# Optimization experiments

Measured on AMD Instinct MI355X. Metric: run time of the kernel, lower is better.

The kernel has to match this reference:

```python
import jax, jax.numpy as jnp
import numpy as np

N_NODES = 100000
HIDDEN = 256
N_MOVES = 500000
N_GRAPHS = 512
EPS = 1e-16  # matches pyg softmax denominator eps


def setup_inputs() -> dict:
    key = jax.random.key(0)
    k1, k2, k3, k4, k5, k6, k7 = jax.random.split(key, 7)
    node_embeddings = jax.random.normal(k1, (N_NODES, HIDDEN), dtype=jnp.float32)
    legal_moves = jax.random.randint(k2, (2, N_MOVES), 0, N_NODES, dtype=jnp.int64)
    batch = jnp.sort(jax.random.randint(k3, (N_NODES,), 0, N_GRAPHS, dtype=jnp.int64))
    # MLP params: Linear(2h, h) -> ReLU -> Linear(h, 1)
    s1 = 1.0 / np.sqrt(2 * HIDDEN)
    s2 = 1.0 / np.sqrt(HIDDEN)
    W1 = jax.random.uniform(k4, (2 * HIDDEN, HIDDEN), jnp.float32, -s1, s1)
    b1 = jax.random.uniform(k5, (HIDDEN,), jnp.float32, -s1, s1)
    W2 = jax.random.uniform(k6, (HIDDEN, 1), jnp.float32, -s2, s2)
    b2 = jax.random.uniform(k7, (1,), jnp.float32, -s2, s2)
    return {"node_embeddings": node_embeddings, "legal_moves": legal_moves,
            "batch": batch, "W1": W1, "b1": b1, "W2": W2, "b2": b2}


def reference(node_embeddings, legal_moves, batch, W1, b1, W2, b2):
    sources = legal_moves[0]
    targets = legal_moves[1]
    # gather endpoints and concat -> [E, 2h]
    move_features = jnp.concatenate(
        [node_embeddings[sources], node_embeddings[targets]], axis=-1)
    h = jax.nn.relu(move_features @ W1 + b1)          # [E, h]
    logits = jnp.squeeze(h @ W2 + b2, axis=-1)        # [E]
    # segment softmax over the graph each move's source node belongs to
    move_batch = batch[sources]                        # [E]
    seg_max = jax.ops.segment_max(logits, move_batch, num_segments=N_GRAPHS)
    ex = jnp.exp(logits - seg_max[move_batch])
    seg_sum = jax.ops.segment_sum(ex, move_batch, num_segments=N_GRAPHS)
    probs = ex / (seg_sum[move_batch] + EPS)
    return probs
```

## Files before the change

### kernel.cpp

```cpp
#include <hip/hip_runtime.h>
#include <hip/hip_bf16.h>

#define NNODES 100000
#define HID 256
#define NMOVES 500000
#define NGRAPHS 512
#define BM 128
#define BN 32
#define PB 128

typedef __attribute__((ext_vector_type(8))) short short8;
typedef __attribute__((ext_vector_type(4))) float f32x4;

#define AS_GLOBAL __attribute__((address_space(1)))
#define AS_LDS __attribute__((address_space(3)))

__device__ __forceinline__ unsigned f2bf(float f) {
    unsigned u = __builtin_bit_cast(unsigned, f);
    u += 0x7FFFu + ((u >> 16) & 1u);
    return u >> 16;
}
__device__ __forceinline__ float bf2f(ushort h) {
    unsigned u = ((unsigned)h) << 16;
    return __builtin_bit_cast(float, u);
}
__device__ __forceinline__ unsigned encf(float f) {
    unsigned b = __builtin_bit_cast(unsigned, f);
    return (b & 0x80000000u) ? ~b : (b ^ 0x80000000u);
}
__device__ __forceinline__ float decf(unsigned u) {
    unsigned b = (u & 0x80000000u) ? (u ^ 0x80000000u) : ~u;
    return __builtin_bit_cast(float, b);
}

__global__ void k_convert_w1(const float* __restrict__ W1, ushort* __restrict__ W1t) {
    int t = blockIdx.x * blockDim.x + threadIdx.x;
    int n = t >> 8, k = t & 255;
    float v = (n < 256) ? W1[k * 256 + n] : W1[(k + 256) * 256 + (n - 256)];
    W1t[t] = (ushort)f2bf(v);
}

__global__ __launch_bounds__(512, 4) void k_gemm(const float* __restrict__ emb,
                                                 const ushort* __restrict__ Bt,
                                                 ushort* __restrict__ P, int M) {
    __shared__ __align__(16) char lds[65536];
    int tid = threadIdx.x;
    int lane = tid & 63;
    int wave = tid >> 6;
    int tm = blockIdx.x * BM;
    int wm = wave >> 1;
    int wn = wave & 1;
    int fr = lane & 15;
    int q = lane >> 4;
    int sw = fr & 7;

#pragma unroll
    for (int i = 0; i < 8; ++i) {
        int cid = i * 512 + tid;
        int row = cid >> 5;
        int j = cid & 31;
        int grow = tm + row; if (grow >= M) grow = M - 1;
        const float4* sp = reinterpret_cast<const float4*>(emb + (size_t)grow * 256 + (j << 3));
        float4 v0 = sp[0], v1 = sp[1];
        uint4 o;
        o.x = f2bf(v0.x) | (f2bf(v0.y) << 16);
        o.y = f2bf(v0.z) | (f2bf(v0.w) << 16);
        o.z = f2bf(v1.x) | (f2bf(v1.y) << 16);
        o.w = f2bf(v1.z) | (f2bf(v1.w) << 16);
        *reinterpret_cast<uint4*>(lds + row * 512 + ((j ^ (row & 7)) << 4)) = o;
    }
    __syncthreads();

    short8 af[2][8];
#pragma unroll
    for (int m = 0; m < 2; ++m) {
        int row = wm * 32 + m * 16 + fr;
#pragma unroll
        for (int kt = 0; kt < 8; ++kt)
            af[m][kt] = *reinterpret_cast<const short8*>(
                lds + row * 512 + (((kt * 4 + q) ^ sw) << 4));
    }
    __syncthreads();

#define STAGE(STRIP, BUFI)                                                          \
    {                                                                               \
        int tn2 = (STRIP) * BN;                                                     \
        _Pragma("unroll")                                                           \
        for (int i = 0; i < 2; ++i) {                                               \
            int cid = i * 512 + tid;                                                \
            int row = cid >> 5, c = cid & 31;                                       \
            const ushort* src = Bt + (size_t)(tn2 + row) * 256 + ((c ^ (row & 7)) << 3); \
            __builtin_amdgcn_global_load_lds((const AS_GLOBAL void*)src,            \
                (AS_LDS void*)(lds + (BUFI) * 16384 + (i * 512 + wave * 64) * 16),  \
                16, 0, 0);                                                          \
        }                                                                           \
    }

    STAGE(0, 0);
    STAGE(1, 1);

#pragma unroll 1
    for (int r = 0; r < 16; ++r) {
        if (r == 0)      asm volatile("s_waitcnt vmcnt(2)" ::: "memory");
        else if (r < 15) asm volatile("s_waitcnt vmcnt(10)" ::: "memory");
        else             asm volatile("s_waitcnt vmcnt(8)" ::: "memory");
        asm volatile("s_barrier" ::: "memory");

        const char* bp = lds + (r & 1) * 16384;
        f32x4 acc0 = {0.f, 0.f, 0.f, 0.f};
        f32x4 acc1 = {0.f, 0.f, 0.f, 0.f};
#pragma unroll
        for (int kt = 0; kt < 8; ++kt) {
            short8 bf = *reinterpret_cast<const short8*>(
                bp + (wn * 16 + fr) * 512 + (((kt * 4 + q) ^ sw) << 4));
            acc0 = __builtin_amdgcn_mfma_f32_16x16x32_bf16(af[0][kt], bf, acc0, 0, 0, 0);
            acc1 = __builtin_amdgcn_mfma_f32_16x16x32_bf16(af[1][kt], bf, acc1, 0, 0, 0);
        }
        int pcol = r * BN + wn * 16 + fr;
#pragma unroll
        for (int j = 0; j < 4; ++j) {
            int prow0 = tm + wm * 32 + q * 4 + j;
            if (prow0 < M) P[(size_t)prow0 * 512 + pcol] = (ushort)f2bf(acc0[j]);
            int prow1 = prow0 + 16;
            if (prow1 < M) P[(size_t)prow1 * 512 + pcol] = (ushort)f2bf(acc1[j]);
        }

        asm volatile("s_barrier" ::: "memory");
        if (r < 14) STAGE(r + 2, (r & 1));
    }
#undef STAGE
}

__device__ __forceinline__ float dot8(uint4 a, uint4 b, const float* b1v, const float* w2v, int o) {
    unsigned aw[4] = {a.x, a.y, a.z, a.w};
    unsigned bw[4] = {b.x, b.y, b.z, b.w};
    float r = 0.f;
#pragma unroll
    for (int i = 0; i < 4; ++i) {
        float a0 = bf2f((ushort)(aw[i] & 0xffffu));
        float a1 = bf2f((ushort)(aw[i] >> 16));
        float c0 = bf2f((ushort)(bw[i] & 0xffffu));
        float c1 = bf2f((ushort)(bw[i] >> 16));
        float h0 = fmaxf(a0 + c0 + b1v[o + 2 * i], 0.f);
        float h1 = fmaxf(a1 + c1 + b1v[o + 2 * i + 1], 0.f);
        r += h0 * w2v[o + 2 * i] + h1 * w2v[o + 2 * i + 1];
    }
    return r;
}

__global__ __launch_bounds__(256) void k_moves(const int* __restrict__ srcs,
                                               const int* __restrict__ tgts,
                                               const int* __restrict__ batch,
                                               const ushort* __restrict__ P,
                                               const float* __restrict__ b1,
                                               const float* __restrict__ W2,
                                               const float* __restrict__ b2,
                                               float* __restrict__ logits,
                                               int* __restrict__ mb) {
    int tid = threadIdx.x;
    int lane = tid & 63;
    int sub = lane >> 4;
    int ch = lane & 15;

    float b1v[16], w2v[16];
    const float4* b1p = reinterpret_cast<const float4*>(b1);
    const float4* w2p = reinterpret_cast<const float4*>(W2);
#pragma unroll
    for (int q = 0; q < 4; ++q) {
        float4 bv = b1p[ch * 4 + q];
        float4 wv = w2p[ch * 4 + q];
        b1v[q * 4 + 0] = bv.x; b1v[q * 4 + 1] = bv.y; b1v[q * 4 + 2] = bv.z; b1v[q * 4 + 3] = bv.w;
        w2v[q * 4 + 0] = wv.x; w2v[q * 4 + 1] = wv.y; w2v[q * 4 + 2] = wv.z; w2v[q * 4 + 3] = wv.w;
    }
    float b2s = b2[0];

    int wid = (blockIdx.x * 256 + tid) >> 6;
    int nw = (gridDim.x * 256) >> 6;

    for (int base = wid * 8; base < NMOVES; base += nw * 8) {
        int m0 = base + sub;
        int m1 = base + 4 + sub;
        int s0 = srcs[m0], t0 = tgts[m0];
        int s1 = srcs[m1], t1 = tgts[m1];
        const uint4* pa0 = reinterpret_cast<const uint4*>(P + (size_t)s0 * 512 + ch * 16);
        const uint4* pb0 = reinterpret_cast<const uint4*>(P + (size_t)t0 * 512 + 256 + ch * 16);
        const uint4* pa1 = reinterpret_cast<const uint4*>(P + (size_t)s1 * 512 + ch * 16);
        const uint4* pb1 = reinterpret_cast<const uint4*>(P + (size_t)t1 * 512 + 256 + ch * 16);
        uint4 a00 = pa0[0], a01 = pa0[1];
        uint4 c00 = pb0[0], c01 = pb0[1];
        uint4 a10 = pa1[0], a11 = pa1[1];
        uint4 c10 = pb1[0], c11 = pb1[1];
        int g0 = batch[s0];
        int g1 = batch[s1];

        float p0 = dot8(a00, c00, b1v, w2v, 0) + dot8(a01, c01, b1v, w2v, 8);
        float p1 = dot8(a10, c10, b1v, w2v, 0) + dot8(a11, c11, b1v, w2v, 8);
#pragma unroll
        for (int off = 1; off < 16; off <<= 1) {
            p0 += __shfl_xor(p0, off);
            p1 += __shfl_xor(p1, off);
        }
        if (ch == 0) {
            logits[m0] = p0 + b2s; mb[m0] = g0;
            logits[m1] = p1 + b2s; mb[m1] = g1;
        }
    }
}

__global__ __launch_bounds__(256) void k_part(const float* __restrict__ logits,
                                              const int* __restrict__ mb,
                                              float* __restrict__ pmax,
                                              float* __restrict__ psum) {
    __shared__ unsigned lmax[NGRAPHS];
    __shared__ float lsum[NGRAPHS];
    int tid = threadIdx.x;
    lmax[tid] = 0u; lmax[tid + 256] = 0u;
    lsum[tid] = 0.f; lsum[tid + 256] = 0.f;
    __syncthreads();

    const int NV = NMOVES / 4;
    int stride = PB * 256;
    for (int v = blockIdx.x * 256 + tid; v < NV; v += stride) {
        float4 l = reinterpret_cast<const float4*>(logits)[v];
        int4 g = reinterpret_cast<const int4*>(mb)[v];
        atomicMax(&lmax[g.x], encf(l.x));
        atomicMax(&lmax[g.y], encf(l.y));
        atomicMax(&lmax[g.z], encf(l.z));
        atomicMax(&lmax[g.w], encf(l.w));
    }
    __syncthreads();
    for (int v = blockIdx.x * 256 + tid; v < NV; v += stride) {
        float4 l = reinterpret_cast<const float4*>(logits)[v];
        int4 g = reinterpret_cast<const int4*>(mb)[v];
        atomicAdd(&lsum[g.x], __expf(l.x - decf(lmax[g.x])));
        atomicAdd(&lsum[g.y], __expf(l.y - decf(lmax[g.y])));
        atomicAdd(&lsum[g.z], __expf(l.z - decf(lmax[g.z])));
        atomicAdd(&lsum[g.w], __expf(l.w - decf(lmax[g.w])));
    }
    __syncthreads();

#pragma unroll
    for (int i = 0; i < 2; ++i) {
        int s = tid + i * 256;
        unsigned e = lmax[s];
        pmax[blockIdx.x * NGRAPHS + s] = (e == 0u) ? -INFINITY : decf(e);
        psum[blockIdx.x * NGRAPHS + s] = lsum[s];
    }
}

__global__ __launch_bounds__(64) void k_combine(const float* __restrict__ pmax,
                                                const float* __restrict__ psum,
                                                float* __restrict__ gmax,
                                                float* __restrict__ ginv) {
    int s = blockIdx.x;
    int lane = threadIdx.x;
    float pm0 = pmax[lane * NGRAPHS + s];
    float pm1 = pmax[(lane + 64) * NGRAPHS + s];
    float ps0 = psum[lane * NGRAPHS + s];
    float ps1 = psum[(lane + 64) * NGRAPHS + s];
    float M = fmaxf(pm0, pm1);
#pragma unroll
    for (int off = 32; off; off >>= 1) M = fmaxf(M, __shfl_xor(M, off));
    float S = (ps0 > 0.f ? ps0 * __expf(pm0 - M) : 0.f)
            + (ps1 > 0.f ? ps1 * __expf(pm1 - M) : 0.f);
#pragma unroll
    for (int off = 32; off; off >>= 1) S += __shfl_xor(S, off);
    if (lane == 0) {
        gmax[s] = M;
        ginv[s] = 1.f / (S + 1e-16f);
    }
}

__global__ void k_norm(const float* __restrict__ logits, const int* __restrict__ mb,
                       const float* __restrict__ gmax, const float* __restrict__ ginv,
                       float* __restrict__ out) {
    const int NV = NMOVES / 4;
    int i = blockIdx.x * blockDim.x + threadIdx.x;
    int n = gridDim.x * blockDim.x;
    for (int v = i; v < NV; v += n) {
        float4 l = reinterpret_cast<const float4*>(logits)[v];
        int4 g = reinterpret_cast<const int4*>(mb)[v];
        float4 o;
        o.x = __expf(l.x - gmax[g.x]) * ginv[g.x];
        o.y = __expf(l.y - gmax[g.y]) * ginv[g.y];
        o.z = __expf(l.z - gmax[g.z]) * ginv[g.z];
        o.w = __expf(l.w - gmax[g.w]) * ginv[g.w];
        reinterpret_cast<float4*>(out)[v] = o;
    }
}

extern "C" void kernel_launch(void* const* d_in, const int* in_sizes, int n_in,
                              void* d_out, int out_size, void* d_ws, size_t ws_size,
                              hipStream_t stream) {
    const float* emb = (const float*)d_in[0];
    const int* moves = (const int*)d_in[1];
    const int* batch = (const int*)d_in[2];
    const float* W1 = (const float*)d_in[3];
    const float* b1 = (const float*)d_in[4];
    const float* W2 = (const float*)d_in[5];
    const float* b2 = (const float*)d_in[6];
    float* out = (float*)d_out;

    auto al = [](size_t x) { return (x + 255) & ~(size_t)255; };
    char* ws = (char*)d_ws;
    size_t off = 0;
    ushort* W1t = (ushort*)(ws + off); off += al((size_t)512 * 256 * 2);
    ushort* P   = (ushort*)(ws + off); off += al((size_t)NNODES * 512 * 2);
    float* logits = (float*)(ws + off); off += al((size_t)NMOVES * 4);
    int* mb       = (int*)(ws + off);   off += al((size_t)NMOVES * 4);
    float* pmax   = (float*)(ws + off); off += al((size_t)PB * NGRAPHS * 4);
    float* psum   = (float*)(ws + off); off += al((size_t)PB * NGRAPHS * 4);
    float* gmax   = (float*)(ws + off); off += al((size_t)NGRAPHS * 4);
    float* ginv   = (float*)(ws + off); off += al((size_t)NGRAPHS * 4);

    k_convert_w1<<<512, 256, 0, stream>>>(W1, W1t);

    int tiles_m = (NNODES + BM - 1) / BM;
    k_gemm<<<tiles_m, 512, 0, stream>>>(emb, W1t, P, NNODES);

    k_moves<<<2048, 256, 0, stream>>>(moves, moves + NMOVES, batch, P, b1, W2, b2,
                                      logits, mb);
    k_part<<<PB, 256, 0, stream>>>(logits, mb, pmax, psum);
    k_combine<<<NGRAPHS, 64, 0, stream>>>(pmax, psum, gmax, ginv);
    k_norm<<<512, 256, 0, stream>>>(logits, mb, gmax, ginv, out);
}
```

Before: 146.9 us.

## Restage GEMM with 128-wide B strips, register-loaded A, and packed transposed stores

```diff
diff --git a/kernel.cpp b/kernel.cpp
--- a/kernel.cpp
+++ b/kernel.cpp
@@ -6,7 +6,6 @@
 #define NMOVES 500000
 #define NGRAPHS 512
 #define BM 128
-#define BN 32
 #define PB 128
 
 typedef __attribute__((ext_vector_type(8))) short short8;
@@ -40,10 +39,10 @@
     W1t[t] = (ushort)f2bf(v);
 }
 
-__global__ __launch_bounds__(512, 4) void k_gemm(const float* __restrict__ emb,
+__global__ __launch_bounds__(512, 2) void k_gemm(const float* __restrict__ emb,
                                                  const ushort* __restrict__ Bt,
                                                  ushort* __restrict__ P, int M) {
-    __shared__ __align__(16) char lds[65536];
+    __shared__ __align__(16) char lds[131072];
     int tid = threadIdx.x;
     int lane = tid & 63;
     int wave = tid >> 6;
@@ -54,80 +53,108 @@
     int q = lane >> 4;
     int sw = fr & 7;
 
-#pragma unroll
-    for (int i = 0; i < 8; ++i) {
-        int cid = i * 512 + tid;
-        int row = cid >> 5;
-        int j = cid & 31;
-        int grow = tm + row; if (grow >= M) grow = M - 1;
-        const float4* sp = reinterpret_cast<const float4*>(emb + (size_t)grow * 256 + (j << 3));
-        float4 v0 = sp[0], v1 = sp[1];
-        uint4 o;
-        o.x = f2bf(v0.x) | (f2bf(v0.y) << 16);
-        o.y = f2bf(v0.z) | (f2bf(v0.w) << 16);
-        o.z = f2bf(v1.x) | (f2bf(v1.y) << 16);
-        o.w = f2bf(v1.z) | (f2bf(v1.w) << 16);
-        *reinterpret_cast<uint4*>(lds + row * 512 + ((j ^ (row & 7)) << 4)) = o;
-    }
-    __syncthreads();
-
-    short8 af[2][8];
-#pragma unroll
-    for (int m = 0; m < 2; ++m) {
-        int row = wm * 32 + m * 16 + fr;
-#pragma unroll
-        for (int kt = 0; kt < 8; ++kt)
-            af[m][kt] = *reinterpret_cast<const short8*>(
-                lds + row * 512 + (((kt * 4 + q) ^ sw) << 4));
-    }
-    __syncthreads();
-
 #define STAGE(STRIP, BUFI)                                                          \
     {                                                                               \
-        int tn2 = (STRIP) * BN;                                                     \
         _Pragma("unroll")                                                           \
-        for (int i = 0; i < 2; ++i) {                                               \
-            int cid = i * 512 + tid;                                                \
+        for (int i = 0; i < 8; ++i) {                                               \
+            int cid = i * 512 + tid;                         \
             int row = cid >> 5, c = cid & 31;                                       \
-            const ushort* src = Bt + (size_t)(tn2 + row) * 256 + ((c ^ (row & 7)) << 3); \
+            const ushort* src = Bt + (size_t)((STRIP) * 128 + row) * 256            \
+                                   + ((c ^ (row & 7)) << 3);                        \
             __builtin_amdgcn_global_load_lds((const AS_GLOBAL void*)src,            \
-                (AS_LDS void*)(lds + (BUFI) * 16384 + (i * 512 + wave * 64) * 16),  \
-                16, 0, 0);                                                          \
+                (AS_LDS void*)(lds + (BUFI) * 65536 + cid * 16), 16, 0, 0);         \
         }                                                                           \
     }
 
     STAGE(0, 0);
     STAGE(1, 1);
 
-#pragma unroll 1
-    for (int r = 0; r < 16; ++r) {
-        if (r == 0)      asm volatile("s_waitcnt vmcnt(2)" ::: "memory");
-        else if (r < 15) asm volatile("s_waitcnt vmcnt(10)" ::: "memory");
-        else             asm volatile("s_waitcnt vmcnt(8)" ::: "memory");
-        asm volatile("s_barrier" ::: "memory");
-
-        const char* bp = lds + (r & 1) * 16384;
-        f32x4 acc0 = {0.f, 0.f, 0.f, 0.f};
-        f32x4 acc1 = {0.f, 0.f, 0.f, 0.f};
+    short8 af[2][8];
+#pragma unroll
+    for (int m = 0; m < 2; ++m) {
+        int grow = tm + wm * 32 + m * 16 + fr;
+        if (grow >= M) grow = M - 1;
+        const float* base = emb + (size_t)grow * 256;
 #pragma unroll
         for (int kt = 0; kt < 8; ++kt) {
-            short8 bf = *reinterpret_cast<const short8*>(
-                bp + (wn * 16 + fr) * 512 + (((kt * 4 + q) ^ sw) << 4));
-            acc0 = __builtin_amdgcn_mfma_f32_16x16x32_bf16(af[0][kt], bf, acc0, 0, 0, 0);
-            acc1 = __builtin_amdgcn_mfma_f32_16x16x32_bf16(af[1][kt], bf, acc1, 0, 0, 0);
+            float4 v0 = *reinterpret_cast<const float4*>(base + (kt * 4 + q) * 8);
+            float4 v1 = *reinterpret_cast<const float4*>(base + (kt * 4 + q) * 8 + 4);
+            short8 f;
+            f[0] = (short)f2bf(v0.x); f[1] = (short)f2bf(v0.y);
+            f[2] = (short)f2bf(v0.z); f[3] = (short)f2bf(v0.w);
+            f[4] = (short)f2bf(v1.x); f[5] = (short)f2bf(v1.y);
+            f[6] = (short)f2bf(v1.z); f[7] = (short)f2bf(v1.w);
+            af[m][kt] = f;
         }
-        int pcol = r * BN + wn * 16 + fr;
-#pragma unroll
-        for (int j = 0; j < 4; ++j) {
-            int prow0 = tm + wm * 32 + q * 4 + j;
-            if (prow0 < M) P[(size_t)prow0 * 512 + pcol] = (ushort)f2bf(acc0[j]);
-            int prow1 = prow0 + 16;
-            if (prow1 < M) P[(size_t)prow1 * 512 + pcol] = (ushort)f2bf(acc1[j]);
+    }
+
+    f32x4 acc[4][4][2];
+#pragma unroll
+    for (int r = 0; r < 4; ++r)
+#pragma unroll
+        for (int n = 0; n < 4; ++n)
+#pragma unroll
+            for (int m = 0; m < 2; ++m) acc[r][n][m] = (f32x4){0.f, 0.f, 0.f, 0.f};
+
+#define STRIP_COMPUTE(R)                                                            \
+    {                                                                               \
+        const char* bp = lds + ((R) & 1) * 65536;                                   \
+        _Pragma("unroll")                                                           \
+        for (int kt = 0; kt < 8; ++kt) {                                            \
+            short8 bf[4];                                                           \
+            _Pragma("unroll")                                                       \
+            for (int n = 0; n < 4; ++n)                                             \
+                bf[n] = *reinterpret_cast<const short8*>(                           \
+                    bp + (wn * 64 + n * 16 + fr) * 512 + (((kt * 4 + q) ^ sw) << 4)); \
+            _Pragma("unroll")                                                       \
+            for (int n = 0; n < 4; ++n) {                                           \
+                acc[R][n][0] = __builtin_amdgcn_mfma_f32_16x16x32_bf16(             \
+                    bf[n], af[0][kt], acc[R][n][0], 0, 0, 0);                       \
+                acc[R][n][1] = __builtin_amdgcn_mfma_f32_16x16x32_bf16(             \
+                    bf[n], af[1][kt], acc[R][n][1], 0, 0, 0);                       \
+            }                                                                       \
+        }                                                                           \
+    }
+
+    asm volatile("s_waitcnt vmcnt(8)" ::: "memory");
+    asm volatile("s_barrier" ::: "memory");
+    STRIP_COMPUTE(0);
+    asm volatile("s_barrier" ::: "memory");
+    STAGE(2, 0);
+
+    asm volatile("s_waitcnt vmcnt(8)" ::: "memory");
+    asm volatile("s_barrier" ::: "memory");
+    STRIP_COMPUTE(1);
+    asm volatile("s_barrier" ::: "memory");
+    STAGE(3, 1);
+
+    asm volatile("s_waitcnt vmcnt(8)" ::: "memory");
+    asm volatile("s_barrier" ::: "memory");
+    STRIP_COMPUTE(2);
+    asm volatile("s_barrier" ::: "memory");
+
+    asm volatile("s_waitcnt vmcnt(0)" ::: "memory");
+    asm volatile("s_barrier" ::: "memory");
+    STRIP_COMPUTE(3);
+
+#pragma unroll
+    for (int r = 0; r < 4; ++r) {
+#pragma unroll
+        for (int m = 0; m < 2; ++m) {
+            int prow = tm + wm * 32 + m * 16 + fr;
+            if (prow < M) {
+#pragma unroll
+                for (int n = 0; n < 4; ++n) {
+                    int pcol = r * 128 + wn * 64 + n * 16 + q * 4;
+                    uint2 pk;
+                    pk.x = f2bf(acc[r][n][m][0]) | (f2bf(acc[r][n][m][1]) << 16);
+                    pk.y = f2bf(acc[r][n][m][2]) | (f2bf(acc[r][n][m][3]) << 16);
+                    *reinterpret_cast<uint2*>(P + (size_t)prow * 512 + pcol) = pk;
+                }
+            }
         }
-
-        asm volatile("s_barrier" ::: "memory");
-        if (r < 14) STAGE(r + 2, (r & 1));
-    }
+    }
+#undef STRIP_COMPUTE
 #undef STAGE
 }
 
```

New measurement: 184.6 us. 1.26x slower.

## Load A fragments directly from global, halve LDS, swap MFMA operands for packed stores

Applied to the files above, without the earlier changes.

```diff
diff --git a/kernel.cpp b/kernel.cpp
--- a/kernel.cpp
+++ b/kernel.cpp
@@ -40,10 +40,10 @@
     W1t[t] = (ushort)f2bf(v);
 }
 
-__global__ __launch_bounds__(512, 4) void k_gemm(const float* __restrict__ emb,
+__global__ __launch_bounds__(512, 8) void k_gemm(const float* __restrict__ emb,
                                                  const ushort* __restrict__ Bt,
                                                  ushort* __restrict__ P, int M) {
-    __shared__ __align__(16) char lds[65536];
+    __shared__ __align__(16) char lds[32768];
     int tid = threadIdx.x;
     int lane = tid & 63;
     int wave = tid >> 6;
@@ -54,42 +54,14 @@
     int q = lane >> 4;
     int sw = fr & 7;
 
-#pragma unroll
-    for (int i = 0; i < 8; ++i) {
-        int cid = i * 512 + tid;
-        int row = cid >> 5;
-        int j = cid & 31;
-        int grow = tm + row; if (grow >= M) grow = M - 1;
-        const float4* sp = reinterpret_cast<const float4*>(emb + (size_t)grow * 256 + (j << 3));
-        float4 v0 = sp[0], v1 = sp[1];
-        uint4 o;
-        o.x = f2bf(v0.x) | (f2bf(v0.y) << 16);
-        o.y = f2bf(v0.z) | (f2bf(v0.w) << 16);
-        o.z = f2bf(v1.x) | (f2bf(v1.y) << 16);
-        o.w = f2bf(v1.z) | (f2bf(v1.w) << 16);
-        *reinterpret_cast<uint4*>(lds + row * 512 + ((j ^ (row & 7)) << 4)) = o;
-    }
-    __syncthreads();
-
-    short8 af[2][8];
-#pragma unroll
-    for (int m = 0; m < 2; ++m) {
-        int row = wm * 32 + m * 16 + fr;
-#pragma unroll
-        for (int kt = 0; kt < 8; ++kt)
-            af[m][kt] = *reinterpret_cast<const short8*>(
-                lds + row * 512 + (((kt * 4 + q) ^ sw) << 4));
-    }
-    __syncthreads();
-
 #define STAGE(STRIP, BUFI)                                                          \
     {                                                                               \
-        int tn2 = (STRIP) * BN;                                                     \
         _Pragma("unroll")                                                           \
         for (int i = 0; i < 2; ++i) {                                               \
-            int cid = i * 512 + tid;                                                \
+            int cid = i * 512 + tid;                         \
             int row = cid >> 5, c = cid & 31;                                       \
-            const ushort* src = Bt + (size_t)(tn2 + row) * 256 + ((c ^ (row & 7)) << 3); \
+            const ushort* src = Bt + (size_t)((STRIP) * BN + row) * 256             \
+                                   + ((c ^ (row & 7)) << 3);                        \
             __builtin_amdgcn_global_load_lds((const AS_GLOBAL void*)src,            \
                 (AS_LDS void*)(lds + (BUFI) * 16384 + (i * 512 + wave * 64) * 16),  \
                 16, 0, 0);                                                          \
@@ -99,11 +71,29 @@
     STAGE(0, 0);
     STAGE(1, 1);
 
+    short8 af[2][8];
+#pragma unroll
+    for (int m = 0; m < 2; ++m) {
+        int grow = tm + wm * 32 + m * 16 + fr;
+        if (grow >= M) grow = M - 1;
+        const float* base = emb + (size_t)grow * 256;
+#pragma unroll
+        for (int kt = 0; kt < 8; ++kt) {
+            float4 v0 = *reinterpret_cast<const float4*>(base + (kt * 4 + q) * 8);
+            float4 v1 = *reinterpret_cast<const float4*>(base + (kt * 4 + q) * 8 + 4);
+            short8 f;
+            f[0] = (short)f2bf(v0.x); f[1] = (short)f2bf(v0.y);
+            f[2] = (short)f2bf(v0.z); f[3] = (short)f2bf(v0.w);
+            f[4] = (short)f2bf(v1.x); f[5] = (short)f2bf(v1.y);
+            f[6] = (short)f2bf(v1.z); f[7] = (short)f2bf(v1.w);
+            af[m][kt] = f;
+        }
+    }
+
 #pragma unroll 1
     for (int r = 0; r < 16; ++r) {
-        if (r == 0)      asm volatile("s_waitcnt vmcnt(2)" ::: "memory");
-        else if (r < 15) asm volatile("s_waitcnt vmcnt(10)" ::: "memory");
-        else             asm volatile("s_waitcnt vmcnt(8)" ::: "memory");
+        if (r < 15) asm volatile("s_waitcnt vmcnt(4)" ::: "memory");
+        else        asm volatile("s_waitcnt vmcnt(2)" ::: "memory");
         asm volatile("s_barrier" ::: "memory");
 
         const char* bp = lds + (r & 1) * 16384;
@@ -113,16 +103,23 @@
         for (int kt = 0; kt < 8; ++kt) {
             short8 bf = *reinterpret_cast<const short8*>(
                 bp + (wn * 16 + fr) * 512 + (((kt * 4 + q) ^ sw) << 4));
-            acc0 = __builtin_amdgcn_mfma_f32_16x16x32_bf16(af[0][kt], bf, acc0, 0, 0, 0);
-            acc1 = __builtin_amdgcn_mfma_f32_16x16x32_bf16(af[1][kt], bf, acc1, 0, 0, 0);
-        }
-        int pcol = r * BN + wn * 16 + fr;
-#pragma unroll
-        for (int j = 0; j < 4; ++j) {
-            int prow0 = tm + wm * 32 + q * 4 + j;
-            if (prow0 < M) P[(size_t)prow0 * 512 + pcol] = (ushort)f2bf(acc0[j]);
-            int prow1 = prow0 + 16;
-            if (prow1 < M) P[(size_t)prow1 * 512 + pcol] = (ushort)f2bf(acc1[j]);
+            acc0 = __builtin_amdgcn_mfma_f32_16x16x32_bf16(bf, af[0][kt], acc0, 0, 0, 0);
+            acc1 = __builtin_amdgcn_mfma_f32_16x16x32_bf16(bf, af[1][kt], acc1, 0, 0, 0);
+        }
+        int pcol = r * BN + wn * 16 + q * 4;
+        int prow0 = tm + wm * 32 + fr;
+        if (prow0 < M) {
+            uint2 pk;
+            pk.x = f2bf(acc0[0]) | (f2bf(acc0[1]) << 16);
+            pk.y = f2bf(acc0[2]) | (f2bf(acc0[3]) << 16);
+            *reinterpret_cast<uint2*>(P + (size_t)prow0 * 512 + pcol) = pk;
+        }
+        int prow1 = prow0 + 16;
+        if (prow1 < M) {
+            uint2 pk;
+            pk.x = f2bf(acc1[0]) | (f2bf(acc1[1]) << 16);
+            pk.y = f2bf(acc1[2]) | (f2bf(acc1[3]) << 16);
+            *reinterpret_cast<uint2*>(P + (size_t)prow1 * 512 + pcol) = pk;
         }
 
         asm volatile("s_barrier" ::: "memory");
```

After: 362.9 us. +147.1%, slower.

## Fuse per-block segment max/sum partials into move-logit kernel, drop k_part

Applied to the files above, without the earlier changes.

```diff
diff --git a/kernel.cpp b/kernel.cpp
--- a/kernel.cpp
+++ b/kernel.cpp
@@ -7,7 +7,7 @@
 #define NGRAPHS 512
 #define BM 128
 #define BN 32
-#define PB 128
+#define PBM 2048
 
 typedef __attribute__((ext_vector_type(8))) short short8;
 typedef __attribute__((ext_vector_type(4))) float f32x4;
@@ -84,12 +84,12 @@
 
 #define STAGE(STRIP, BUFI)                                                          \
     {                                                                               \
-        int tn2 = (STRIP) * BN;                                                     \
         _Pragma("unroll")                                                           \
         for (int i = 0; i < 2; ++i) {                                               \
-            int cid = i * 512 + tid;                                                \
+            int cid = i * 512 + tid;                         \
             int row = cid >> 5, c = cid & 31;                                       \
-            const ushort* src = Bt + (size_t)(tn2 + row) * 256 + ((c ^ (row & 7)) << 3); \
+            const ushort* src = Bt + (size_t)((STRIP) * BN + row) * 256             \
+                                   + ((c ^ (row & 7)) << 3);                        \
             __builtin_amdgcn_global_load_lds((const AS_GLOBAL void*)src,            \
                 (AS_LDS void*)(lds + (BUFI) * 16384 + (i * 512 + wave * 64) * 16),  \
                 16, 0, 0);                                                          \
@@ -156,11 +156,18 @@
                                                const float* __restrict__ W2,
                                                const float* __restrict__ b2,
                                                float* __restrict__ logits,
-                                               int* __restrict__ mb) {
+                                               int* __restrict__ mb,
+                                               float* __restrict__ pmax,
+                                               float* __restrict__ psum) {
+    __shared__ unsigned lmax[NGRAPHS];
+    __shared__ float lsum[NGRAPHS];
     int tid = threadIdx.x;
     int lane = tid & 63;
     int sub = lane >> 4;
     int ch = lane & 15;
+    lmax[tid] = 0u; lmax[tid + 256] = 0u;
+    lsum[tid] = 0.f; lsum[tid + 256] = 0.f;
+    __syncthreads();
 
     float b1v[16], w2v[16];
     const float4* b1p = reinterpret_cast<const float4*>(b1);
@@ -201,41 +208,21 @@
             p1 += __shfl_xor(p1, off);
         }
         if (ch == 0) {
-            logits[m0] = p0 + b2s; mb[m0] = g0;
-            logits[m1] = p1 + b2s; mb[m1] = g1;
-        }
-    }
-}
-
-__global__ __launch_bounds__(256) void k_part(const float* __restrict__ logits,
-                                              const int* __restrict__ mb,
-                                              float* __restrict__ pmax,
-                                              float* __restrict__ psum) {
-    __shared__ unsigned lmax[NGRAPHS];
-    __shared__ float lsum[NGRAPHS];
-    int tid = threadIdx.x;
-    lmax[tid] = 0u; lmax[tid + 256] = 0u;
-    lsum[tid] = 0.f; lsum[tid + 256] = 0.f;
-    __syncthreads();
-
-    const int NV = NMOVES / 4;
-    int stride = PB * 256;
-    for (int v = blockIdx.x * 256 + tid; v < NV; v += stride) {
-        float4 l = reinterpret_cast<const float4*>(logits)[v];
-        int4 g = reinterpret_cast<const int4*>(mb)[v];
-        atomicMax(&lmax[g.x], encf(l.x));
-        atomicMax(&lmax[g.y], encf(l.y));
-        atomicMax(&lmax[g.z], encf(l.z));
-        atomicMax(&lmax[g.w], encf(l.w));
-    }
-    __syncthreads();
-    for (int v = blockIdx.x * 256 + tid; v < NV; v += stride) {
-        float4 l = reinterpret_cast<const float4*>(logits)[v];
-        int4 g = reinterpret_cast<const int4*>(mb)[v];
-        atomicAdd(&lsum[g.x], __expf(l.x - decf(lmax[g.x])));
-        atomicAdd(&lsum[g.y], __expf(l.y - decf(lmax[g.y])));
-        atomicAdd(&lsum[g.z], __expf(l.z - decf(lmax[g.z])));
-        atomicAdd(&lsum[g.w], __expf(l.w - decf(lmax[g.w])));
+            float l0 = p0 + b2s;
+            float l1 = p1 + b2s;
+            logits[m0] = l0; mb[m0] = g0; atomicMax(&lmax[g0], encf(l0));
+            logits[m1] = l1; mb[m1] = g1; atomicMax(&lmax[g1], encf(l1));
+        }
+    }
+    __syncthreads();
+
+    {
+        int m = wid * 8 + (lane >> 3) * (nw * 8) + (lane & 7);
+        if (m < NMOVES) {
+            float l = logits[m];
+            int g = mb[m];
+            atomicAdd(&lsum[g], __expf(l - decf(lmax[g])));
+        }
     }
     __syncthreads();
 
@@ -243,29 +230,46 @@
     for (int i = 0; i < 2; ++i) {
         int s = tid + i * 256;
         unsigned e = lmax[s];
-        pmax[blockIdx.x * NGRAPHS + s] = (e == 0u) ? -INFINITY : decf(e);
-        psum[blockIdx.x * NGRAPHS + s] = lsum[s];
-    }
-}
-
-__global__ __launch_bounds__(64) void k_combine(const float* __restrict__ pmax,
-                                                const float* __restrict__ psum,
-                                                float* __restrict__ gmax,
-                                                float* __restrict__ ginv) {
+        pmax[(size_t)blockIdx.x * NGRAPHS + s] = (e == 0u) ? -INFINITY : decf(e);
+        psum[(size_t)blockIdx.x * NGRAPHS + s] = lsum[s];
+    }
+}
+
+__global__ __launch_bounds__(256) void k_combine(const float* __restrict__ pmax,
+                                                 const float* __restrict__ psum,
+                                                 float* __restrict__ gmax,
+                                                 float* __restrict__ ginv) {
+    __shared__ float wred[8];
     int s = blockIdx.x;
-    int lane = threadIdx.x;
-    float pm0 = pmax[lane * NGRAPHS + s];
-    float pm1 = pmax[(lane + 64) * NGRAPHS + s];
-    float ps0 = psum[lane * NGRAPHS + s];
-    float ps1 = psum[(lane + 64) * NGRAPHS + s];
-    float M = fmaxf(pm0, pm1);
+    int tid = threadIdx.x;
+    int lane = tid & 63;
+    int wave = tid >> 6;
+
+    float pm[8], ps[8];
+#pragma unroll
+    for (int i = 0; i < 8; ++i) {
+        pm[i] = pmax[(size_t)(tid + 256 * i) * NGRAPHS + s];
+        ps[i] = psum[(size_t)(tid + 256 * i) * NGRAPHS + s];
+    }
+    float M = pm[0];
+#pragma unroll
+    for (int i = 1; i < 8; ++i) M = fmaxf(M, pm[i]);
 #pragma unroll
     for (int off = 32; off; off >>= 1) M = fmaxf(M, __shfl_xor(M, off));
-    float S = (ps0 > 0.f ? ps0 * __expf(pm0 - M) : 0.f)
-            + (ps1 > 0.f ? ps1 * __expf(pm1 - M) : 0.f);
+    if (lane == 0) wred[wave] = M;
+    __syncthreads();
+    M = fmaxf(fmaxf(wred[0], wred[1]), fmaxf(wred[2], wred[3]));
+
+    float S = 0.f;
+#pragma unroll
+    for (int i = 0; i < 8; ++i)
+        if (ps[i] > 0.f) S += ps[i] * __expf(pm[i] - M);
 #pragma unroll
     for (int off = 32; off; off >>= 1) S += __shfl_xor(S, off);
-    if (lane == 0) {
+    if (lane == 0) wred[4 + wave] = S;
+    __syncthreads();
+    if (tid == 0) {
+        S = wred[4] + wred[5] + wred[6] + wred[7];
         gmax[s] = M;
         ginv[s] = 1.f / (S + 1e-16f);
     }
@@ -308,8 +312,8 @@
     ushort* P   = (ushort*)(ws + off); off += al((size_t)NNODES * 512 * 2);
     float* logits = (float*)(ws + off); off += al((size_t)NMOVES * 4);
     int* mb       = (int*)(ws + off);   off += al((size_t)NMOVES * 4);
-    float* pmax   = (float*)(ws + off); off += al((size_t)PB * NGRAPHS * 4);
-    float* psum   = (float*)(ws + off); off += al((size_t)PB * NGRAPHS * 4);
+    float* pmax   = (float*)(ws + off); off += al((size_t)PBM * NGRAPHS * 4);
+    float* psum   = (float*)(ws + off); off += al((size_t)PBM * NGRAPHS * 4);
     float* gmax   = (float*)(ws + off); off += al((size_t)NGRAPHS * 4);
     float* ginv   = (float*)(ws + off); off += al((size_t)NGRAPHS * 4);
 
@@ -318,9 +322,8 @@
     int tiles_m = (NNODES + BM - 1) / BM;
     k_gemm<<<tiles_m, 512, 0, stream>>>(emb, W1t, P, NNODES);
 
-    k_moves<<<2048, 256, 0, stream>>>(moves, moves + NMOVES, batch, P, b1, W2, b2,
-                                      logits, mb);
-    k_part<<<PB, 256, 0, stream>>>(logits, mb, pmax, psum);
-    k_combine<<<NGRAPHS, 64, 0, stream>>>(pmax, psum, gmax, ginv);
+    k_moves<<<PBM, 256, 0, stream>>>(moves, moves + NMOVES, batch, P, b1, W2, b2,
+                                     logits, mb, pmax, psum);
+    k_combine<<<NGRAPHS, 256, 0, stream>>>(pmax, psum, gmax, ginv);
     k_norm<<<512, 256, 0, stream>>>(logits, mb, gmax, ginv, out);
 }
```

After: 153.4 us. 1.04x slower.
